# Optimization experiments

Measured on AMD Instinct MI355X. Metric: run time of the kernel, lower is better.

The kernel has to match this reference:

```python
import jax, jax.numpy as jnp
import numpy as np
import math

H = 16
D_MODEL = 1024
D_K = D_MODEL // H


def setup_inputs() -> dict:
    key0 = jax.random.key(0)
    ks = jax.random.split(key0, 20)
    B, S, D = 4, 1024, D_MODEL
    inp = {
        'query': jax.random.normal(ks[0], (B, S, D), jnp.float32),
        'key': jax.random.normal(ks[1], (B, S, D), jnp.float32),
        'value': jax.random.normal(ks[2], (B, S, D), jnp.float32),
        'mask': jnp.ones((B, 1, S), jnp.int32),
    }
    sc = 1.0 / math.sqrt(D)
    # linears[0]=key proj, [1]=value proj, [2]=query proj, [3]=output proj (per source)
    names = ['W_k', 'W_v', 'W_q', 'W_o', 'W_fq', 'W_fg']
    for i, n in enumerate(names):
        inp[n] = jax.random.normal(ks[3 + i], (D, D), jnp.float32) * sc
        inp['b' + n[1:]] = jnp.zeros((D,), jnp.float32)
    inp['up'] = jax.random.normal(ks[10], (H, 1, D_K), jnp.float32) * sc
    inp['uz'] = jax.random.normal(ks[11], (H, 1, D_K), jnp.float32) * sc
    return inp


def _heads(x, B, S):
    return jnp.transpose(x.reshape(B, S, H, D_K), (0, 2, 1, 3))  # [B,h,S,d_k]


def reference(query, key, value, mask, W_k, b_k, W_v, b_v, W_q, b_q, W_o, b_o, W_fq, b_fq, W_fg, b_fg, up, uz):
    B, S, D = query.shape
    k = _heads(key @ W_k.T + b_k, B, S)
    v = _heads(value @ W_v.T + b_v, B, S)
    q_lin = query @ W_q.T + b_q  # [B,S,D]
    # Gaussian focus bias
    glo = jnp.mean(q_lin, axis=1, keepdims=True)  # [B,1,D]
    c = jnp.tanh(q_lin @ W_fq.T + b_fq + (glo @ W_fg.T + b_fg))
    c = _heads(c, B, S)  # [B,h,S,d_k]
    p = jnp.sum(c * up, axis=-1)  # [B,h,S]
    z = jnp.sum(c * uz, axis=-1)
    P = jax.nn.sigmoid(p) * S
    Z = jax.nn.sigmoid(z) * S
    j = jnp.arange(S, dtype=P.dtype)  # key positions
    G = -((j[None, None, None, :] - P[..., None]) ** 2) * 2.0 / (Z[..., None] ** 2)  # [B,h,S,S]
    q = _heads(q_lin, B, S)
    scores = jnp.einsum('bhqd,bhkd->bhqk', q, k) / math.sqrt(D_K) + G
    scores = jnp.where(mask[:, None] == 0, jnp.float32(-1e15), scores)
    attn = jax.nn.softmax(scores, axis=-1)
    x = jnp.einsum('bhqk,bhkd->bhqd', attn, v)
    x = jnp.transpose(x, (0, 2, 1, 3)).reshape(B, S, D)
    out = x @ W_o.T + b_o
    return out, jnp.mean(attn, axis=1)
```

## Files before the change

kernel.cpp:

```cpp
#include <hip/hip_runtime.h>
#include <hip/hip_bf16.h>
#include <math.h>

typedef __attribute__((ext_vector_type(8))) short short8;
typedef __attribute__((ext_vector_type(4))) short short4v;
typedef __attribute__((ext_vector_type(4))) float f32x4;
typedef unsigned short u16;

#define SC2 0.18033688011112042f
#define L2E 1.4426950408889634f

__device__ __forceinline__ u16 f2bf(float f) {
  union { float f; unsigned u; } v; v.f = f;
  unsigned u = v.u + 0x7fffu + ((v.u >> 16) & 1u);
  return (u16)(u >> 16);
}
__device__ __forceinline__ float bf2f(u16 h) {
  union { unsigned u; float f; } v; v.u = ((unsigned)h) << 16;
  return v.f;
}
__device__ __forceinline__ float fexp2(float x) {
  float r; asm("v_exp_f32 %0, %1" : "=v"(r) : "v"(x)); return r;
}
__device__ __forceinline__ void gl_lds16(const u16* g, u16* l) {
  __builtin_amdgcn_global_load_lds(
      (const __attribute__((address_space(1))) void*)g,
      (__attribute__((address_space(3))) void*)l, 16, 0, 0);
}

__device__ __forceinline__ size_t KFoff(int b, int h, int j, int d) {
  return ((((size_t)(b * 16 + h) * 64 + (j >> 4)) * 3 + (d >> 5)) * 64
          + ((d >> 3) & 3) * 16 + (j & 15)) * 8 + (d & 7);
}
__device__ __forceinline__ size_t VFoff(int b, int h, int j, int d) {
  return ((((size_t)(b * 16 + h) * 4 + (d >> 4)) * 32 + (j >> 5)) * 64
          + ((j >> 3) & 3) * 16 + (d & 15)) * 8 + (j & 7);
}

__global__ __launch_bounds__(256) void cvt_all(
    const float* __restrict__ q, const float* __restrict__ k, const float* __restrict__ v,
    const float* __restrict__ w0, const float* __restrict__ w1, const float* __restrict__ w2,
    const float* __restrict__ w3, const float* __restrict__ w4,
    u16* __restrict__ qb, u16* __restrict__ kb, u16* __restrict__ vb,
    u16* __restrict__ w0b, u16* __restrict__ w1b, u16* __restrict__ w2b,
    u16* __restrict__ w3b, u16* __restrict__ w4b,
    const int* __restrict__ mask, u16* __restrict__ Kf) {
  int bid = blockIdx.x;
  if (bid >= 8704) {
    int bidx = bid - 8704;
    int b = bidx >> 6, jt = bidx & 63;
    int t = threadIdx.x;
    int h = t >> 4, jj = t & 15;
    int j = jt * 16 + jj;
    float jc = (float)(j - 512);
    float mbv = (mask[b * 1024 + j] == 0) ? -1.4e15f : 0.0f;
    u16* base = Kf + ((size_t)((b * 16 + h) * 64 + jt) * 3 + 2) * 512;
    short8 z8 = (short8){0, 0, 0, 0, 0, 0, 0, 0};
    short8 f8 = z8;
    f8[0] = (short)f2bf(jc * jc);
    f8[1] = (short)f2bf(jc);
    f8[2] = (short)f2bf(1.0f);
    f8[3] = (short)f2bf(mbv);
    *(short8*)(base + jj * 8) = f8;
    *(short8*)(base + 128 + jj * 8) = z8;
    *(short8*)(base + 256 + jj * 8) = z8;
    *(short8*)(base + 384 + jj * 8) = z8;
    return;
  }
  const float* s; u16* d; int base;
  if (bid < 2048)      { s = q; d = qb; base = bid; }
  else if (bid < 4096) { s = k; d = kb; base = bid - 2048; }
  else if (bid < 6144) { s = v; d = vb; base = bid - 4096; }
  else {
    int t2 = bid - 6144; int wi = t2 >> 9; base = t2 & 511;
    if (wi == 0)      { s = w0; d = w0b; }
    else if (wi == 1) { s = w1; d = w1b; }
    else if (wi == 2) { s = w2; d = w2b; }
    else if (wi == 3) { s = w3; d = w3b; }
    else              { s = w4; d = w4b; }
  }
  size_t idx = (size_t)base * 2048 + (size_t)threadIdx.x * 8;
  float4 a = *(const float4*)(s + idx);
  float4 b = *(const float4*)(s + idx + 4);
  short8 o;
  o[0] = (short)f2bf(a.x); o[1] = (short)f2bf(a.y); o[2] = (short)f2bf(a.z); o[3] = (short)f2bf(a.w);
  o[4] = (short)f2bf(b.x); o[5] = (short)f2bf(b.y); o[6] = (short)f2bf(b.z); o[7] = (short)f2bf(b.w);
  *(short8*)(d + idx) = o;
}

#define GEMM_CORE(A_, Bw_)                                                              \
  f32x4 acc[4][4];                                                                      \
  _Pragma("unroll") for (int m = 0; m < 4; ++m)                                         \
    _Pragma("unroll") for (int n = 0; n < 4; ++n)                                       \
      acc[m][n] = (f32x4){0.f, 0.f, 0.f, 0.f};                                          \
  for (int k0 = 0; k0 < 1024; k0 += 64) {                                               \
    _Pragma("unroll") for (int p = 0; p < 4; ++p) {                                     \
      int idx = p * 256 + tid;                                                          \
      int row = idx >> 3, slot = idx & 7;                                               \
      gl_lds16(A_ + (size_t)(m0 + row) * 1024 + k0 + ((slot ^ (row & 7)) * 8), As + idx * 8); \
    }                                                                                   \
    _Pragma("unroll") for (int p = 0; p < 4; ++p) {                                     \
      int idx = p * 256 + tid;                                                          \
      int row = idx >> 3, slot = idx & 7;                                               \
      gl_lds16(Bw_ + (size_t)(n0 + row) * 1024 + k0 + ((slot ^ (row & 7)) * 8), Bs + idx * 8); \
    }                                                                                   \
    __syncthreads();                                                                    \
    _Pragma("unroll") for (int kk = 0; kk < 2; ++kk) {                                  \
      short8 af[4], bf[4];                                                              \
      _Pragma("unroll") for (int m = 0; m < 4; ++m) {                                   \
        int row = wrow + m * 16 + c;                                                    \
        af[m] = *(const short8*)(As + row * 64 + (((kk * 4 + g) ^ (row & 7)) * 8));     \
      }                                                                                 \
      _Pragma("unroll") for (int n = 0; n < 4; ++n) {                                   \
        int row = wcol + n * 16 + c;                                                    \
        bf[n] = *(const short8*)(Bs + row * 64 + (((kk * 4 + g) ^ (row & 7)) * 8));     \
      }                                                                                 \
      _Pragma("unroll") for (int m = 0; m < 4; ++m)                                     \
        _Pragma("unroll") for (int n = 0; n < 4; ++n)                                   \
          acc[m][n] = __builtin_amdgcn_mfma_f32_16x16x32_bf16(af[m], bf[n], acc[m][n], 0, 0, 0); \
    }                                                                                   \
    __syncthreads();                                                                    \
  }

__global__ __launch_bounds__(256, 2)
void proj_qkv(const u16* __restrict__ qb, const u16* __restrict__ kb, const u16* __restrict__ vb,
              const u16* __restrict__ wqb, const u16* __restrict__ wkb, const u16* __restrict__ wvb,
              const float* __restrict__ bq, const float* __restrict__ bk, const float* __restrict__ bv,
              u16* __restrict__ Ql, u16* __restrict__ Kf, u16* __restrict__ Vf) {
  __shared__ u16 As[128 * 64];
  __shared__ u16 Bs[128 * 64];
  const int z = blockIdx.z;
  const u16* A  = (z == 0) ? kb : (z == 1) ? vb : qb;
  const u16* Bw = (z == 0) ? wkb : (z == 1) ? wvb : wqb;
  const float* bias = (z == 0) ? bk : (z == 1) ? bv : bq;
  const int tid = threadIdx.x;
  const int l = tid & 63, w = tid >> 6;
  const int m0 = blockIdx.x * 128, n0 = blockIdx.y * 128;
  const int wrow = (w & 1) * 64, wcol = (w >> 1) * 64;
  const int g = l >> 4, c = l & 15;

  GEMM_CORE(A, Bw)

#pragma unroll
  for (int n = 0; n < 4; ++n) {
    int col = n0 + wcol + n * 16 + c;
    float bv_ = bias[col];
    int hh = col >> 6, dd = col & 63;
#pragma unroll
    for (int m = 0; m < 4; ++m) {
#pragma unroll
      for (int r = 0; r < 4; ++r) {
        int rowg = m0 + wrow + m * 16 + g * 4 + r;
        float val = acc[m][n][r] + bv_;
        int bb = rowg >> 10, jj = rowg & 1023;
        if (z == 0)      Kf[KFoff(bb, hh, jj, dd)] = f2bf(val * SC2);
        else if (z == 1) Vf[VFoff(bb, hh, jj, dd)] = f2bf(val);
        else             Ql[(size_t)rowg * 1024 + col] = f2bf(val);
      }
    }
  }
}

__global__ __launch_bounds__(256, 2)
void gemm_tanh_pz(const u16* __restrict__ A, const u16* __restrict__ Bw,
                  const float* __restrict__ gb,
                  const float* __restrict__ up, const float* __restrict__ uz,
                  float* __restrict__ Pout, float* __restrict__ IZout) {
  __shared__ u16 As[128 * 64];
  __shared__ u16 Bs[128 * 64];
  const int tid = threadIdx.x;
  const int l = tid & 63, w = tid >> 6;
  const int m0 = blockIdx.x * 128, n0 = blockIdx.y * 128;
  const int wrow = (w & 1) * 64, wcol = (w >> 1) * 64;
  const int g = l >> 4, c = l & 15;

  GEMM_CORE(A, Bw)

  const int hglob = (n0 + wcol) >> 6;
  const int batch = m0 >> 10;
  float upv[4], uzv[4], gbv[4];
#pragma unroll
  for (int n = 0; n < 4; ++n) {
    int col = n0 + wcol + n * 16 + c;
    upv[n] = up[col];
    uzv[n] = uz[col];
    gbv[n] = gb[batch * 1024 + col];
  }
#pragma unroll
  for (int m = 0; m < 4; ++m) {
#pragma unroll
    for (int r = 0; r < 4; ++r) {
      float pp = 0.f, zz = 0.f;
#pragma unroll
      for (int n = 0; n < 4; ++n) {
        float cval = tanhf(acc[m][n][r] + gbv[n]);
        pp += cval * upv[n];
        zz += cval * uzv[n];
      }
#pragma unroll
      for (int d = 1; d < 16; d <<= 1) {
        pp += __shfl_xor(pp, d);
        zz += __shfl_xor(zz, d);
      }
      if (c == 0) {
        int rowg = m0 + wrow + m * 16 + g * 4 + r;
        int qi = rowg & 1023;
        float Pv = 1024.f / (1.f + __expf(-pp));
        float Zv = 1024.f / (1.f + __expf(-zz));
        size_t o = (size_t)(batch * 16 + hglob) * 1024 + qi;
        Pout[o] = Pv;
        IZout[o] = 2.0f / (Zv * Zv) * L2E;
      }
    }
  }
}

__global__ __launch_bounds__(128) void glo_part_k(const u16* __restrict__ qlin, float* __restrict__ gpart) {
  int b = blockIdx.x & 3, seg = blockIdx.x >> 2;
  int t = threadIdx.x;
  float acc[8] = {0, 0, 0, 0, 0, 0, 0, 0};
  for (int s = seg * 16; s < seg * 16 + 16; ++s) {
    short8 v = *(const short8*)(qlin + (size_t)(b * 1024 + s) * 1024 + t * 8);
#pragma unroll
    for (int j = 0; j < 8; ++j) acc[j] += bf2f((u16)v[j]);
  }
#pragma unroll
  for (int j = 0; j < 8; ++j) gpart[(size_t)(seg * 4 + b) * 1024 + t * 8 + j] = acc[j];
}

__global__ __launch_bounds__(128) void glo_reduce(const float* __restrict__ gpart, float* __restrict__ glo) {
  int b = blockIdx.x & 3, cc = blockIdx.x >> 2;
  int col = cc * 128 + threadIdx.x;
  float a[8] = {0, 0, 0, 0, 0, 0, 0, 0};
#pragma unroll
  for (int s8 = 0; s8 < 8; ++s8) {
#pragma unroll
    for (int s = 0; s < 8; ++s)
      a[s] += gpart[(size_t)((s8 * 8 + s) * 4 + b) * 1024 + col];
  }
  float t = ((a[0] + a[1]) + (a[2] + a[3])) + ((a[4] + a[5]) + (a[6] + a[7]));
  glo[b * 1024 + col] = t * (1.0f / 1024.0f);
}

__global__ __launch_bounds__(256) void gbias_k(const float* __restrict__ glo, const float* __restrict__ Wfg,
                                               const float* __restrict__ bfq, const float* __restrict__ bfg,
                                               float* __restrict__ gbias) {
  __shared__ float glo_l[4096];
  int tid = threadIdx.x;
  for (int idx = tid; idx < 4096; idx += 256) glo_l[idx] = glo[idx];
  __syncthreads();
  int w = tid >> 6, l = tid & 63;
#pragma unroll
  for (int i = 0; i < 4; ++i) {
    int n = blockIdx.x * 16 + w * 4 + i;
    float a0 = 0, a1 = 0, a2 = 0, a3 = 0;
#pragma unroll
    for (int kk = 0; kk < 4; ++kk) {
      int k = kk * 256 + l * 4;
      float4 wv = *(const float4*)(Wfg + (size_t)n * 1024 + k);
      float4 g0 = *(const float4*)(&glo_l[k]);
      float4 g1 = *(const float4*)(&glo_l[1024 + k]);
      float4 g2 = *(const float4*)(&glo_l[2048 + k]);
      float4 g3 = *(const float4*)(&glo_l[3072 + k]);
      a0 += wv.x * g0.x + wv.y * g0.y + wv.z * g0.z + wv.w * g0.w;
      a1 += wv.x * g1.x + wv.y * g1.y + wv.z * g1.z + wv.w * g1.w;
      a2 += wv.x * g2.x + wv.y * g2.y + wv.z * g2.z + wv.w * g2.w;
      a3 += wv.x * g3.x + wv.y * g3.y + wv.z * g3.z + wv.w * g3.w;
    }
#pragma unroll
    for (int d = 1; d < 64; d <<= 1) {
      a0 += __shfl_xor(a0, d); a1 += __shfl_xor(a1, d);
      a2 += __shfl_xor(a2, d); a3 += __shfl_xor(a3, d);
    }
    if (l == 0) {
      float bb = bfq[n] + bfg[n];
      gbias[n] = a0 + bb; gbias[1024 + n] = a1 + bb;
      gbias[2048 + n] = a2 + bb; gbias[3072 + n] = a3 + bb;
    }
  }
}

template<int WP>
__global__ __launch_bounds__(512, 4)
void attn_flash(const u16* __restrict__ Qlin, const u16* __restrict__ Kf, const u16* __restrict__ Vf,
                const float* __restrict__ Pbuf, const float* __restrict__ IZbuf,
                u16* __restrict__ xbuf, float* __restrict__ Mbuf, float* __restrict__ iLbuf,
                u16* __restrict__ Pall, float* __restrict__ mch) {
  __shared__ u16 sm16[28672];

  const int tid = threadIdx.x;
  const int l = tid & 63, w = tid >> 6;
  const int g = l >> 4, c = l & 15;
  const int bid = blockIdx.x;
  const int bh = (bid & 7) + ((bid >> 6) << 3);
  const int qc = (bid >> 3) & 7;
  const int b = bh >> 4, h = bh & 15;
  const int q0w = qc * 128 + w * 16;

  char* ps_ = (char*)(sm16 + 20480) + w * 2048;

  const u16* KfH = Kf + (size_t)bh * 98304;
  const u16* VfH = Vf + (size_t)bh * 65536;

  const u16* qrow = Qlin + (size_t)(b * 1024 + q0w + c) * 1024 + h * 64 + g * 8;
  short8 af0 = *(const short8*)qrow;
  short8 af1 = *(const short8*)(qrow + 32);
  short8 af2 = (short8){0, 0, 0, 0, 0, 0, 0, 0};
  if (g == 0) {
    float Pc = Pbuf[(size_t)bh * 1024 + q0w + c] - 512.0f;
    float Ic = IZbuf[(size_t)bh * 1024 + q0w + c];
    af2[0] = (short)f2bf(-Ic);
    af2[1] = (short)f2bf(2.0f * Pc * Ic);
    af2[2] = (short)f2bf(-Pc * Pc * Ic);
    af2[3] = (short)f2bf(1.0f);
  }

  float m[4], lsum[4];
  f32x4 xacc[4];
#pragma unroll
  for (int r = 0; r < 4; ++r) { m[r] = -3.0e38f; lsum[r] = 0.f; }
#pragma unroll
  for (int dt = 0; dt < 4; ++dt) xacc[dt] = (f32x4){0.f, 0.f, 0.f, 0.f};

  auto stage = [&](int jn, u16* nb) {
    gl_lds16(KfH + (size_t)jn * 6144 + tid * 8, nb + tid * 8);
    if (tid < 256) {
      gl_lds16(KfH + (size_t)jn * 6144 + (512 + tid) * 8, nb + (512 + tid) * 8);
      int v = tid + 256;
      gl_lds16(VfH + ((size_t)((v >> 7) * 32 + jn * 2) * 512) + (v & 127) * 8, nb + 6144 + v * 8);
    } else {
      int v = tid - 256;
      gl_lds16(VfH + ((size_t)((v >> 7) * 32 + jn * 2) * 512) + (v & 127) * 8, nb + 6144 + v * 8);
    }
  };

  stage(0, sm16);
  __syncthreads();

  for (int jc = 0; jc < 16; ++jc) {
    const int bi = jc & 1;
    u16* Ksb = sm16 + bi * 10240;
    u16* Vsb = Ksb + 6144;
    if (jc < 15) stage(jc + 1, sm16 + (bi ^ 1) * 10240);

    f32x4 sc[4];
    float cm[4] = {-3.0e38f, -3.0e38f, -3.0e38f, -3.0e38f};
    __builtin_amdgcn_s_setprio(1);
#pragma unroll
    for (int t = 0; t < 4; ++t) {
      short8 b0 = *(const short8*)(Ksb + (t * 3 + 0) * 512 + l * 8);
      short8 b1 = *(const short8*)(Ksb + (t * 3 + 1) * 512 + l * 8);
      short8 b2 = *(const short8*)(Ksb + (t * 3 + 2) * 512 + l * 8);
      f32x4 z = (f32x4){0.f, 0.f, 0.f, 0.f};
      z = __builtin_amdgcn_mfma_f32_16x16x32_bf16(af0, b0, z, 0, 0, 0);
      z = __builtin_amdgcn_mfma_f32_16x16x32_bf16(af1, b1, z, 0, 0, 0);
      z = __builtin_amdgcn_mfma_f32_16x16x32_bf16(af2, b2, z, 0, 0, 0);
      sc[t] = z;
#pragma unroll
      for (int r = 0; r < 4; ++r) cm[r] = fmaxf(cm[r], z[r]);
    }
    __builtin_amdgcn_s_setprio(0);
#pragma unroll
    for (int d = 1; d < 16; d <<= 1)
#pragma unroll
      for (int r = 0; r < 4; ++r) cm[r] = fmaxf(cm[r], __shfl_xor(cm[r], d));
    float scale[4], ps[4];
#pragma unroll
    for (int r = 0; r < 4; ++r) {
      float nm = fmaxf(m[r], cm[r]);
      scale[r] = fexp2(m[r] - nm);
      m[r] = nm;
      ps[r] = 0.f;
    }
#pragma unroll
    for (int t = 0; t < 4; ++t) {
#pragma unroll
      for (int r = 0; r < 4; ++r) {
        float p = fexp2(sc[t][r] - m[r]);
        ps[r] += p;
        int row = g * 4 + r;
        int byte = (row * 128 + (t * 16 + c) * 2) ^ ((row & 7) << 4);
        *(u16*)(ps_ + byte) = f2bf(p);
      }
    }
#pragma unroll
    for (int r = 0; r < 4; ++r) {
      lsum[r] = lsum[r] * scale[r] + ps[r];
#pragma unroll
      for (int dt = 0; dt < 4; ++dt) xacc[dt][r] *= scale[r];
    }
    if (WP && c == 0) {
      f32x4 mv;
      mv.x = m[0]; mv.y = m[1]; mv.z = m[2]; mv.w = m[3];
      *(f32x4*)(mch + ((size_t)bh * 16 + jc) * 1024 + q0w + g * 4) = mv;
    }
    if (WP) {
#pragma unroll
      for (int k2 = 0; k2 < 2; ++k2) {
        int i = k2 * 512 + l * 8;
        int row = i >> 6, col = i & 63;
        int byte = (row * 128 + col * 2) ^ ((row & 7) << 4);
        short8 v = *(const short8*)(ps_ + byte);
        *(short8*)(Pall + (((size_t)bh * 16 + jc) * 1024 + q0w + row) * 64 + col) = v;
      }
    }
    short8 pa[2];
#pragma unroll
    for (int ks = 0; ks < 2; ++ks) {
      int abyte = (c * 128 + (ks * 32 + g * 8) * 2) ^ ((c & 7) << 4);
      pa[ks] = *(const short8*)(ps_ + abyte);
    }
    __builtin_amdgcn_s_setprio(1);
#pragma unroll
    for (int dt = 0; dt < 4; ++dt) {
#pragma unroll
      for (int ks = 0; ks < 2; ++ks) {
        short8 vb = *(const short8*)(Vsb + (dt * 2 + ks) * 512 + l * 8);
        xacc[dt] = __builtin_amdgcn_mfma_f32_16x16x32_bf16(pa[ks], vb, xacc[dt], 0, 0, 0);
      }
    }
    __builtin_amdgcn_s_setprio(0);
    if (jc < 15) {
      if (WP) asm volatile("s_waitcnt vmcnt(3)" ::: "memory");
      else    asm volatile("s_waitcnt vmcnt(0)" ::: "memory");
    }
    __builtin_amdgcn_sched_barrier(0);
    __builtin_amdgcn_s_barrier();
    __builtin_amdgcn_sched_barrier(0);
  }

#pragma unroll
  for (int d = 1; d < 16; d <<= 1)
#pragma unroll
    for (int r = 0; r < 4; ++r) lsum[r] += __shfl_xor(lsum[r], d);
  float iLr[4];
#pragma unroll
  for (int r = 0; r < 4; ++r) iLr[r] = 1.0f / lsum[r];
  if (c == 0) {
#pragma unroll
    for (int r = 0; r < 4; ++r) {
      size_t o = (size_t)bh * 1024 + q0w + g * 4 + r;
      Mbuf[o] = m[r];
      iLbuf[o] = iLr[r];
    }
  }
  float* xs = (float*)sm16 + w * 1024;
#pragma unroll
  for (int dt = 0; dt < 4; ++dt)
#pragma unroll
    for (int r = 0; r < 4; ++r)
      xs[(g * 4 + r) * 64 + dt * 16 + c] = xacc[dt][r] * iLr[r];
#pragma unroll
  for (int k2 = 0; k2 < 4; ++k2) {
    int i = k2 * 256 + l * 4;
    int row = i >> 6, d0 = i & 63;
    f32x4 xv = *(const f32x4*)(xs + i);
    short4v o;
    o[0] = (short)f2bf(xv.x); o[1] = (short)f2bf(xv.y);
    o[2] = (short)f2bf(xv.z); o[3] = (short)f2bf(xv.w);
    *(short4v*)(xbuf + (size_t)(b * 1024 + q0w + row) * 1024 + h * 64 + d0) = o;
  }
}

__global__ __launch_bounds__(256, 2)
void epilogue_k(const u16* __restrict__ A, const u16* __restrict__ Bw,
                const float* __restrict__ bias, float* __restrict__ out0,
                const u16* __restrict__ Pall, const float* __restrict__ iLbuf,
                const float* __restrict__ Mbuf, const float* __restrict__ mchb,
                float* __restrict__ out2, int usePall) {
  __shared__ u16 As[128 * 64];
  __shared__ u16 Bs[128 * 64];
  const int bid = blockIdx.x;
  const int tid = threadIdx.x;
  if (bid >= 256) {
    if (!usePall) return;
    int bq = (bid - 256) * 2 + (tid >> 7);
    int b = bq >> 10, q = bq & 1023;
    int j = (tid & 127) * 8;
    int jc = j >> 6, jin = j & 63;
    float acc[8] = {0, 0, 0, 0, 0, 0, 0, 0};
    for (int h = 0; h < 16; ++h) {
      int bh = b * 16 + h;
      float M = Mbuf[(size_t)bh * 1024 + q];
      float iLh = iLbuf[(size_t)bh * 1024 + q];
      float mc = mchb[((size_t)bh * 16 + jc) * 1024 + q];
      float f = fexp2(mc - M) * iLh;
      short8 p = *(const short8*)(Pall + (((size_t)bh * 16 + jc) * 1024 + q) * 64 + jin);
#pragma unroll
      for (int i = 0; i < 8; ++i) acc[i] = fmaf(bf2f((u16)p[i]), f, acc[i]);
    }
    float* dst = out2 + (size_t)bq * 1024 + j;
#pragma unroll
    for (int i = 0; i < 8; ++i) dst[i] = acc[i] * 0.0625f;
    return;
  }
  const int l = tid & 63, w = tid >> 6;
  const int m0 = (bid & 31) * 128, n0 = (bid >> 5) * 128;
  const int wrow = (w & 1) * 64, wcol = (w >> 1) * 64;
  const int g = l >> 4, c = l & 15;

  GEMM_CORE(A, Bw)

#pragma unroll
  for (int n = 0; n < 4; ++n) {
    int col = n0 + wcol + n * 16 + c;
    float bv = bias[col];
#pragma unroll
    for (int m = 0; m < 4; ++m) {
#pragma unroll
      for (int r = 0; r < 4; ++r) {
        int rowg = m0 + wrow + m * 16 + g * 4 + r;
        out0[(size_t)rowg * 1024 + col] = acc[m][n][r] + bv;
      }
    }
  }
}

__global__ __launch_bounds__(512, 4)
void attn_mean(const u16* __restrict__ Qlin, const u16* __restrict__ Kf,
               const float* __restrict__ Pbuf, const float* __restrict__ IZbuf,
               const float* __restrict__ Mbuf, const float* __restrict__ iLbuf,
               const int* __restrict__ mask,
               float* __restrict__ out2) {
  const int tid = threadIdx.x;
  const int l = tid & 63, w = tid >> 6;
  const int g = l >> 4, c = l & 15;
  int chunk = (blockIdx.x % 8) * 64 + blockIdx.x / 8;
  const int b = chunk >> 7;
  const int qt = (chunk & 127) >> 1;
  const int jh = chunk & 1;
  const int q0 = qt * 16;
  const int jbase = jh * 512 + w * 64;

  float mb[4];
#pragma unroll
  for (int t = 0; t < 4; ++t)
    mb[t] = (mask[b * 1024 + jbase + t * 16 + c] == 0) ? -1.4e15f : 0.0f;

  f32x4 macc[4];
#pragma unroll
  for (int t = 0; t < 4; ++t) macc[t] = (f32x4){0.f, 0.f, 0.f, 0.f};

  for (int h = 0; h < 16; ++h) {
    const u16* qrow = Qlin + (size_t)(b * 1024 + q0 + c) * 1024 + h * 64 + g * 8;
    short8 af0 = *(const short8*)qrow;
    short8 af1 = *(const short8*)(qrow + 32);
    const u16* kb2 = Kf + ((size_t)((b * 16 + h) * 64 + jh * 32 + w * 4) * 3) * 512 + l * 8;
    float Pq[4], IZq[4], Mq[4], iLq[4];
#pragma unroll
    for (int r = 0; r < 4; ++r) {
      size_t o = (size_t)(b * 16 + h) * 1024 + q0 + g * 4 + r;
      Pq[r] = Pbuf[o]; IZq[r] = IZbuf[o]; Mq[r] = Mbuf[o]; iLq[r] = iLbuf[o] * 0.0625f;
    }
#pragma unroll
    for (int t = 0; t < 4; ++t) {
      short8 bf0 = *(const short8*)(kb2 + (t * 3 + 0) * 512);
      short8 bf1 = *(const short8*)(kb2 + (t * 3 + 1) * 512);
      f32x4 z = (f32x4){0.f, 0.f, 0.f, 0.f};
      z = __builtin_amdgcn_mfma_f32_16x16x32_bf16(af0, bf0, z, 0, 0, 0);
      z = __builtin_amdgcn_mfma_f32_16x16x32_bf16(af1, bf1, z, 0, 0, 0);
      float jf = (float)(jbase + t * 16 + c);
#pragma unroll
      for (int r = 0; r < 4; ++r) {
        float diff = jf - Pq[r];
        float s = z[r] + mb[t] - diff * diff * IZq[r];
        macc[t][r] += fexp2(s - Mq[r]) * iLq[r];
      }
    }
  }
#pragma unroll
  for (int t = 0; t < 4; ++t) {
#pragma unroll
    for (int r = 0; r < 4; ++r)
      out2[(size_t)(b * 1024 + q0 + g * 4 + r) * 1024 + jbase + t * 16 + c] = macc[t][r];
  }
}

extern "C" void kernel_launch(void* const* d_in, const int* in_sizes, int n_in,
                              void* d_out, int out_size, void* d_ws, size_t ws_size,
                              hipStream_t stream) {
  const float* q   = (const float*)d_in[0];
  const float* k   = (const float*)d_in[1];
  const float* v   = (const float*)d_in[2];
  const int*   msk = (const int*)d_in[3];
  const float* Wk  = (const float*)d_in[4];  const float* bk  = (const float*)d_in[5];
  const float* Wv  = (const float*)d_in[6];  const float* bv  = (const float*)d_in[7];
  const float* Wq  = (const float*)d_in[8];  const float* bq  = (const float*)d_in[9];
  const float* Wo  = (const float*)d_in[10]; const float* bo  = (const float*)d_in[11];
  const float* Wfq = (const float*)d_in[12]; const float* bfq = (const float*)d_in[13];
  const float* Wfg = (const float*)d_in[14]; const float* bfg = (const float*)d_in[15];
  const float* up  = (const float*)d_in[16]; const float* uz  = (const float*)d_in[17];

  const size_t MB = 1u << 20;
  char* base = (char*)d_ws;
  char* p = base;
  auto take = [&](size_t n) { char* r = p; p += (n + 255) & ~(size_t)255; return r; };
  u16* Kf   = (u16*)take(12 * MB);
  u16* Ql   = (u16*)take(8 * MB);
  u16* Vf   = (u16*)take(8 * MB);
  u16* xb   = (u16*)take(8 * MB);
  u16* wob  = (u16*)take(2 * MB);
  float* Pb    = (float*)take((size_t)65536 * 4);
  float* IZb   = (float*)take((size_t)65536 * 4);
  float* Mb    = (float*)take((size_t)65536 * 4);
  float* iLb   = (float*)take((size_t)65536 * 4);
  float* mch   = (float*)take((size_t)64 * 16 * 1024 * 4);
  float* gpart = (float*)take((size_t)64 * 4 * 1024 * 4);
  float* glo   = (float*)take(4096 * 4);
  float* gbias = (float*)take(4096 * 4);
  size_t pool_off = (size_t)(p - base);
  u16* qb   = (u16*)take(8 * MB);
  u16* kb   = (u16*)take(8 * MB);
  u16* vb   = (u16*)take(8 * MB);
  u16* wkb  = (u16*)take(2 * MB);
  u16* wvb  = (u16*)take(2 * MB);
  u16* wqb  = (u16*)take(2 * MB);
  u16* wfqb = (u16*)take(2 * MB);
  u16* Pall = (u16*)(base + pool_off);
  int usePall = (ws_size >= pool_off + (size_t)128 * MB) ? 1 : 0;

  float* out0 = (float*)d_out;
  float* out2 = out0 + (size_t)4 * 1024 * 1024;

  cvt_all<<<8960, 256, 0, stream>>>(q, k, v, Wk, Wv, Wq, Wfq, Wo,
                                    qb, kb, vb, wkb, wvb, wqb, wfqb, wob, msk, Kf);
  dim3 gg3(32, 8, 3);
  proj_qkv<<<gg3, 256, 0, stream>>>(qb, kb, vb, wqb, wkb, wvb, bq, bk, bv, Ql, Kf, Vf);
  dim3 gg(32, 8);
  glo_part_k<<<256, 128, 0, stream>>>(Ql, gpart);
  glo_reduce<<<32, 128, 0, stream>>>(gpart, glo);
  gbias_k<<<64, 256, 0, stream>>>(glo, Wfg, bfq, bfg, gbias);
  gemm_tanh_pz<<<gg, 256, 0, stream>>>(Ql, wfqb, gbias, up, uz, Pb, IZb);
  if (usePall) {
    attn_flash<1><<<512, 512, 0, stream>>>(Ql, Kf, Vf, Pb, IZb, xb, Mb, iLb, Pall, mch);
    epilogue_k<<<2304, 256, 0, stream>>>(xb, wob, bo, out0, Pall, iLb, Mb, mch, out2, 1);
  } else {
    attn_flash<0><<<512, 512, 0, stream>>>(Ql, Kf, Vf, Pb, IZb, xb, Mb, iLb, Pall, mch);
    attn_mean<<<512, 512, 0, stream>>>(Ql, Kf, Pb, IZb, Mb, iLb, msk, out2);
    epilogue_k<<<256, 256, 0, stream>>>(xb, wob, bo, out0, Pall, iLb, Mb, mch, out2, 0);
  }
}
```

Baseline: 186.8 us.

## Generate Gaussian bias K-fragment in registers instead of storing it in Kf

Kf previously held a third 32-wide slice per 16-key tile containing the positional terms (j^2, j, 1, mask bias) that feed the Gaussian-bias MFMA. That slice is now built on the fly in registers inside the attention loop, with the mask bias cached once per block in LDS. This cuts Kf storage and per-tile global-to-LDS traffic by a third, shrinks LDS use, and drops the extra cvt blocks. It also swaps the software bf16 rounding for the hardware packed convert instruction and narrows the s_setprio region; the cost is a few extra ALU ops per tile on the g==0 lanes.

```diff
diff --git a/kernel.cpp b/kernel.cpp
--- a/kernel.cpp
+++ b/kernel.cpp
@@ -15,6 +15,11 @@
   unsigned u = v.u + 0x7fffu + ((v.u >> 16) & 1u);
   return (u16)(u >> 16);
 }
+__device__ __forceinline__ u16 f2bf_fast(float f) {
+  unsigned r;
+  asm("v_cvt_pk_bf16_f32 %0, %1, %2" : "=v"(r) : "v"(f), "v"(f));
+  return (u16)r;
+}
 __device__ __forceinline__ float bf2f(u16 h) {
   union { unsigned u; float f; } v; v.u = ((unsigned)h) << 16;
   return v.f;
@@ -29,7 +34,7 @@
 }
 
 __device__ __forceinline__ size_t KFoff(int b, int h, int j, int d) {
-  return ((((size_t)(b * 16 + h) * 64 + (j >> 4)) * 3 + (d >> 5)) * 64
+  return ((((size_t)(b * 16 + h) * 64 + (j >> 4)) * 2 + (d >> 5)) * 64
           + ((d >> 3) & 3) * 16 + (j & 15)) * 8 + (d & 7);
 }
 __device__ __forceinline__ size_t VFoff(int b, int h, int j, int d) {
@@ -43,30 +48,8 @@
     const float* __restrict__ w3, const float* __restrict__ w4,
     u16* __restrict__ qb, u16* __restrict__ kb, u16* __restrict__ vb,
     u16* __restrict__ w0b, u16* __restrict__ w1b, u16* __restrict__ w2b,
-    u16* __restrict__ w3b, u16* __restrict__ w4b,
-    const int* __restrict__ mask, u16* __restrict__ Kf) {
+    u16* __restrict__ w3b, u16* __restrict__ w4b) {
   int bid = blockIdx.x;
-  if (bid >= 8704) {
-    int bidx = bid - 8704;
-    int b = bidx >> 6, jt = bidx & 63;
-    int t = threadIdx.x;
-    int h = t >> 4, jj = t & 15;
-    int j = jt * 16 + jj;
-    float jc = (float)(j - 512);
-    float mbv = (mask[b * 1024 + j] == 0) ? -1.4e15f : 0.0f;
-    u16* base = Kf + ((size_t)((b * 16 + h) * 64 + jt) * 3 + 2) * 512;
-    short8 z8 = (short8){0, 0, 0, 0, 0, 0, 0, 0};
-    short8 f8 = z8;
-    f8[0] = (short)f2bf(jc * jc);
-    f8[1] = (short)f2bf(jc);
-    f8[2] = (short)f2bf(1.0f);
-    f8[3] = (short)f2bf(mbv);
-    *(short8*)(base + jj * 8) = f8;
-    *(short8*)(base + 128 + jj * 8) = z8;
-    *(short8*)(base + 256 + jj * 8) = z8;
-    *(short8*)(base + 384 + jj * 8) = z8;
-    return;
-  }
   const float* s; u16* d; int base;
   if (bid < 2048)      { s = q; d = qb; base = bid; }
   else if (bid < 4096) { s = k; d = kb; base = bid - 2048; }
@@ -284,9 +267,10 @@
 __global__ __launch_bounds__(512, 4)
 void attn_flash(const u16* __restrict__ Qlin, const u16* __restrict__ Kf, const u16* __restrict__ Vf,
                 const float* __restrict__ Pbuf, const float* __restrict__ IZbuf,
+                const int* __restrict__ mask,
                 u16* __restrict__ xbuf, float* __restrict__ Mbuf, float* __restrict__ iLbuf,
                 u16* __restrict__ Pall, float* __restrict__ mch) {
-  __shared__ u16 sm16[28672];
+  __shared__ u16 sm16[25600];
 
   const int tid = threadIdx.x;
   const int l = tid & 63, w = tid >> 6;
@@ -297,10 +281,14 @@
   const int b = bh >> 4, h = bh & 15;
   const int q0w = qc * 128 + w * 16;
 
-  char* ps_ = (char*)(sm16 + 20480) + w * 2048;
-
-  const u16* KfH = Kf + (size_t)bh * 98304;
+  char* ps_ = (char*)(sm16 + 16384) + w * 2048;
+  u16* maskb_s = sm16 + 24576;
+
+  const u16* KfH = Kf + (size_t)bh * 65536;
   const u16* VfH = Vf + (size_t)bh * 65536;
+
+  for (int i = tid; i < 1024; i += 512)
+    maskb_s[i] = (mask[b * 1024 + i] == 0) ? f2bf(-1.4e15f) : (u16)0;
 
   const u16* qrow = Qlin + (size_t)(b * 1024 + q0w + c) * 1024 + h * 64 + g * 8;
   short8 af0 = *(const short8*)qrow;
@@ -323,15 +311,8 @@
   for (int dt = 0; dt < 4; ++dt) xacc[dt] = (f32x4){0.f, 0.f, 0.f, 0.f};
 
   auto stage = [&](int jn, u16* nb) {
-    gl_lds16(KfH + (size_t)jn * 6144 + tid * 8, nb + tid * 8);
-    if (tid < 256) {
-      gl_lds16(KfH + (size_t)jn * 6144 + (512 + tid) * 8, nb + (512 + tid) * 8);
-      int v = tid + 256;
-      gl_lds16(VfH + ((size_t)((v >> 7) * 32 + jn * 2) * 512) + (v & 127) * 8, nb + 6144 + v * 8);
-    } else {
-      int v = tid - 256;
-      gl_lds16(VfH + ((size_t)((v >> 7) * 32 + jn * 2) * 512) + (v & 127) * 8, nb + 6144 + v * 8);
-    }
+    gl_lds16(KfH + (size_t)jn * 4096 + tid * 8, nb + tid * 8);
+    gl_lds16(VfH + ((size_t)((tid >> 7) * 32 + jn * 2) * 512) + (tid & 127) * 8, nb + 4096 + tid * 8);
   };
 
   stage(0, sm16);
@@ -339,27 +320,35 @@
 
   for (int jc = 0; jc < 16; ++jc) {
     const int bi = jc & 1;
-    u16* Ksb = sm16 + bi * 10240;
-    u16* Vsb = Ksb + 6144;
-    if (jc < 15) stage(jc + 1, sm16 + (bi ^ 1) * 10240);
+    u16* Ksb = sm16 + bi * 8192;
+    u16* Vsb = Ksb + 4096;
+    if (jc < 15) stage(jc + 1, sm16 + (bi ^ 1) * 8192);
 
     f32x4 sc[4];
     float cm[4] = {-3.0e38f, -3.0e38f, -3.0e38f, -3.0e38f};
-    __builtin_amdgcn_s_setprio(1);
 #pragma unroll
     for (int t = 0; t < 4; ++t) {
-      short8 b0 = *(const short8*)(Ksb + (t * 3 + 0) * 512 + l * 8);
-      short8 b1 = *(const short8*)(Ksb + (t * 3 + 1) * 512 + l * 8);
-      short8 b2 = *(const short8*)(Ksb + (t * 3 + 2) * 512 + l * 8);
+      short8 b0 = *(const short8*)(Ksb + (t * 2 + 0) * 512 + l * 8);
+      short8 b1 = *(const short8*)(Ksb + (t * 2 + 1) * 512 + l * 8);
+      short8 b2 = (short8){0, 0, 0, 0, 0, 0, 0, 0};
+      if (g == 0) {
+        int j = jc * 64 + t * 16 + c;
+        float jf = (float)(j - 512);
+        b2[0] = (short)f2bf_fast(jf * jf);
+        b2[1] = (short)f2bf_fast(jf);
+        b2[2] = (short)0x3F80;
+        b2[3] = (short)maskb_s[j];
+      }
+      __builtin_amdgcn_s_setprio(1);
       f32x4 z = (f32x4){0.f, 0.f, 0.f, 0.f};
       z = __builtin_amdgcn_mfma_f32_16x16x32_bf16(af0, b0, z, 0, 0, 0);
       z = __builtin_amdgcn_mfma_f32_16x16x32_bf16(af1, b1, z, 0, 0, 0);
       z = __builtin_amdgcn_mfma_f32_16x16x32_bf16(af2, b2, z, 0, 0, 0);
+      __builtin_amdgcn_s_setprio(0);
       sc[t] = z;
 #pragma unroll
       for (int r = 0; r < 4; ++r) cm[r] = fmaxf(cm[r], z[r]);
     }
-    __builtin_amdgcn_s_setprio(0);
 #pragma unroll
     for (int d = 1; d < 16; d <<= 1)
 #pragma unroll
@@ -380,7 +369,7 @@
         ps[r] += p;
         int row = g * 4 + r;
         int byte = (row * 128 + (t * 16 + c) * 2) ^ ((row & 7) << 4);
-        *(u16*)(ps_ + byte) = f2bf(p);
+        *(u16*)(ps_ + byte) = f2bf_fast(p);
       }
     }
 #pragma unroll
@@ -456,8 +445,8 @@
     int row = i >> 6, d0 = i & 63;
     f32x4 xv = *(const f32x4*)(xs + i);
     short4v o;
-    o[0] = (short)f2bf(xv.x); o[1] = (short)f2bf(xv.y);
-    o[2] = (short)f2bf(xv.z); o[3] = (short)f2bf(xv.w);
+    o[0] = (short)f2bf_fast(xv.x); o[1] = (short)f2bf_fast(xv.y);
+    o[2] = (short)f2bf_fast(xv.z); o[3] = (short)f2bf_fast(xv.w);
     *(short4v*)(xbuf + (size_t)(b * 1024 + q0w + row) * 1024 + h * 64 + d0) = o;
   }
 }
@@ -545,7 +534,7 @@
     const u16* qrow = Qlin + (size_t)(b * 1024 + q0 + c) * 1024 + h * 64 + g * 8;
     short8 af0 = *(const short8*)qrow;
     short8 af1 = *(const short8*)(qrow + 32);
-    const u16* kb2 = Kf + ((size_t)((b * 16 + h) * 64 + jh * 32 + w * 4) * 3) * 512 + l * 8;
+    const u16* kb2 = Kf + ((size_t)((b * 16 + h) * 64 + jh * 32 + w * 4) * 2) * 512 + l * 8;
     float Pq[4], IZq[4], Mq[4], iLq[4];
 #pragma unroll
     for (int r = 0; r < 4; ++r) {
@@ -554,8 +543,8 @@
     }
 #pragma unroll
     for (int t = 0; t < 4; ++t) {
-      short8 bf0 = *(const short8*)(kb2 + (t * 3 + 0) * 512);
-      short8 bf1 = *(const short8*)(kb2 + (t * 3 + 1) * 512);
+      short8 bf0 = *(const short8*)(kb2 + (t * 2 + 0) * 512);
+      short8 bf1 = *(const short8*)(kb2 + (t * 2 + 1) * 512);
       f32x4 z = (f32x4){0.f, 0.f, 0.f, 0.f};
       z = __builtin_amdgcn_mfma_f32_16x16x32_bf16(af0, bf0, z, 0, 0, 0);
       z = __builtin_amdgcn_mfma_f32_16x16x32_bf16(af1, bf1, z, 0, 0, 0);
@@ -595,7 +584,7 @@
   char* base = (char*)d_ws;
   char* p = base;
   auto take = [&](size_t n) { char* r = p; p += (n + 255) & ~(size_t)255; return r; };
-  u16* Kf   = (u16*)take(12 * MB);
+  u16* Kf   = (u16*)take(8 * MB);
   u16* Ql   = (u16*)take(8 * MB);
   u16* Vf   = (u16*)take(8 * MB);
   u16* xb   = (u16*)take(8 * MB);
@@ -622,8 +611,8 @@
   float* out0 = (float*)d_out;
   float* out2 = out0 + (size_t)4 * 1024 * 1024;
 
-  cvt_all<<<8960, 256, 0, stream>>>(q, k, v, Wk, Wv, Wq, Wfq, Wo,
-                                    qb, kb, vb, wkb, wvb, wqb, wfqb, wob, msk, Kf);
+  cvt_all<<<8704, 256, 0, stream>>>(q, k, v, Wk, Wv, Wq, Wfq, Wo,
+                                    qb, kb, vb, wkb, wvb, wqb, wfqb, wob);
   dim3 gg3(32, 8, 3);
   proj_qkv<<<gg3, 256, 0, stream>>>(qb, kb, vb, wqb, wkb, wvb, bq, bk, bv, Ql, Kf, Vf);
   dim3 gg(32, 8);
@@ -632,10 +621,10 @@
   gbias_k<<<64, 256, 0, stream>>>(glo, Wfg, bfq, bfg, gbias);
   gemm_tanh_pz<<<gg, 256, 0, stream>>>(Ql, wfqb, gbias, up, uz, Pb, IZb);
   if (usePall) {
-    attn_flash<1><<<512, 512, 0, stream>>>(Ql, Kf, Vf, Pb, IZb, xb, Mb, iLb, Pall, mch);
+    attn_flash<1><<<512, 512, 0, stream>>>(Ql, Kf, Vf, Pb, IZb, msk, xb, Mb, iLb, Pall, mch);
     epilogue_k<<<2304, 256, 0, stream>>>(xb, wob, bo, out0, Pall, iLb, Mb, mch, out2, 1);
   } else {
-    attn_flash<0><<<512, 512, 0, stream>>>(Ql, Kf, Vf, Pb, IZb, xb, Mb, iLb, Pall, mch);
+    attn_flash<0><<<512, 512, 0, stream>>>(Ql, Kf, Vf, Pb, IZb, msk, xb, Mb, iLb, Pall, mch);
     attn_mean<<<512, 512, 0, stream>>>(Ql, Kf, Pb, IZb, Mb, iLb, msk, out2);
     epilogue_k<<<256, 256, 0, stream>>>(xb, wob, bo, out0, Pall, iLb, Mb, mch, out2, 0);
   }
```

Measured after the change: 186.8 us. About the same (+0.0%).
